# Kernel tuning notes

Measured on AMD Instinct MI355X. Metric: run time of the kernel, lower is better.

## Reference

```python
import jax, jax.numpy as jnp
import numpy as np

N = 6144          # number of agents
D = 2             # spatial dims
BOX = 100.0       # positions spread over [0, BOX)^2
DT = 0.01         # integrator timestep
MASS = 1.0
SOFT = 0.25       # softening added to r^2 to keep LJ r^-12 finite for near-coincident points


def setup_inputs() -> dict:
    key = jax.random.key(0)
    k1, k2, k3, k4 = jax.random.split(key, 4)
    pos = jax.random.uniform(k1, (N, D), dtype=jnp.float32) * BOX
    vel = jax.random.normal(k2, (N, D), dtype=jnp.float32)
    epsilon = jax.random.normal(k3, (), dtype=jnp.float32)
    sigma = jax.random.normal(k4, (), dtype=jnp.float32)
    return {"pos": pos, "vel": vel, "epsilon": epsilon, "sigma": sigma}


def reference(pos, vel, epsilon, sigma):
    # Pairwise Lennard-Jones forces (all-to-all), then one semi-implicit Euler step.
    n = pos.shape[0]
    diff = pos[:, None, :] - pos[None, :, :]          # [N, N, D]
    r2 = jnp.sum(diff * diff, axis=-1)                # [N, N]
    eye = jnp.eye(n, dtype=bool)
    r2s = jnp.where(eye, 1.0, r2 + SOFT)              # avoid div-by-zero on diagonal
    inv_r2 = (sigma * sigma) / r2s                    # (sigma/r)^2
    i6 = inv_r2 * inv_r2 * inv_r2                     # (sigma/r)^6
    # dU/dr of 4*eps*((s/r)^12 - (s/r)^6) -> force coefficient along diff
    coeff = 24.0 * epsilon * (2.0 * i6 * i6 - i6) / r2s
    coeff = jnp.where(eye, 0.0, coeff)                # no self-interaction
    force = jnp.einsum('ij,ijd->id', coeff, diff)     # [N, D]
    vel_new = vel + (DT / MASS) * force
    pos_new = pos + DT * vel_new
    return jnp.concatenate([pos_new, vel_new], axis=-1)  # [N, 2*D] world state
```

## Files before the change

kernel.cpp:

```cpp
#include <hip/hip_runtime.h>

#define NAG   6144
#define DT    0.01f
#define SOFT  0.25f

#define NJS   32
#define IPB   12
#define BLK   (NJS * IPB)
#define NBLK  (NAG / IPB)
#define JITER (NAG / (2 * NJS))

typedef __attribute__((ext_vector_type(2))) float f32x2;

__global__ __launch_bounds__(BLK, 3) void lj_fused(
    const float4* __restrict__ pos4,
    const float2* __restrict__ vel2,
    const float*  __restrict__ eps_p,
    const float*  __restrict__ sig_p,
    float4* __restrict__ out4)
{
    __shared__ __align__(16) float spx[NAG];
    __shared__ __align__(16) float spy[NAG];

    const int tid = threadIdx.x;
    for (int k = tid; k < NAG / 2; k += BLK) {
        const float4 v = pos4[k];
        *(f32x2*)&spx[2 * k] = (f32x2){v.x, v.z};
        *(f32x2*)&spy[2 * k] = (f32x2){v.y, v.w};
    }
    __syncthreads();

    const float eps  = *eps_p, s = *sig_p;
    const float s2   = s * s, s6 = s2 * s2 * s2;
    const float ke   = 24.0f * eps;
    const f32x2 ks12 = (f32x2)(2.0f * ke * s6 * s6);
    const f32x2 mks6 = (f32x2)(-ke * s6);
    const f32x2 softv = (f32x2)(SOFT);

    const int lane  = tid & 63;
    const int js    = lane & (NJS - 1);
    const int i_idx = (tid >> 6) * 2 + (lane >> 5);
    const int i     = blockIdx.x * IPB + i_idx;

    const f32x2 pix = (f32x2)(spx[i]);
    const f32x2 piy = (f32x2)(spy[i]);

    f32x2 fx = 0.f, fy = 0.f;
#pragma unroll 8
    for (int jj = 0; jj < JITER; ++jj) {
        const int j0 = jj * (2 * NJS) + 2 * js;
        const f32x2 xj = *(const f32x2*)&spx[j0];
        const f32x2 yj = *(const f32x2*)&spy[j0];
        const f32x2 dx = pix - xj, dy = piy - yj;
        const f32x2 r  = __builtin_elementwise_fma(dy, dy,
                         __builtin_elementwise_fma(dx, dx, softv));
        f32x2 u;
        u.x = __builtin_amdgcn_rcpf(r.x);
        u.y = __builtin_amdgcn_rcpf(r.y);
        const f32x2 u2 = u * u, u3 = u2 * u, u4 = u2 * u2;
        const f32x2 c  = u4 * __builtin_elementwise_fma(ks12, u3, mks6);
        fx = __builtin_elementwise_fma(c, dx, fx);
        fy = __builtin_elementwise_fma(c, dy, fy);
    }

    float sfx = fx.x + fx.y;
    float sfy = fy.x + fy.y;
#pragma unroll
    for (int m = 16; m >= 1; m >>= 1) {
        sfx += __shfl_xor(sfx, m, 64);
        sfy += __shfl_xor(sfy, m, 64);
    }

    if (js == 0) {
        const float2 v  = vel2[i];
        const float vnx = fmaf(DT, sfx, v.x);
        const float vny = fmaf(DT, sfy, v.y);
        const float pnx = fmaf(DT, vnx, spx[i]);
        const float pny = fmaf(DT, vny, spy[i]);
        out4[i] = make_float4(pnx, pny, vnx, vny);
    }
}

extern "C" void kernel_launch(void* const* d_in, const int* in_sizes, int n_in,
                              void* d_out, int out_size, void* d_ws, size_t ws_size,
                              hipStream_t stream) {
    const float4* pos4  = (const float4*)d_in[0];
    const float2* vel2  = (const float2*)d_in[1];
    const float*  eps_p = (const float*)d_in[2];
    const float*  sig_p = (const float*)d_in[3];
    float4* out4 = (float4*)d_out;
    (void)d_ws; (void)ws_size;

    lj_fused<<<NBLK, BLK, 0, stream>>>(pos4, vel2, eps_p, sig_p, out4);
}
```

Measured before the change: 18.96 us.

## Register-block two i-particles per lane and share one reciprocal per pair

Each 64-lane wavefront now computes forces for two i-agents, with every lane sweeping the full j range. Each j pair loaded from LDS is therefore reused for two i-agents, which halves LDS reads per interaction. The two per-pair reciprocals are also replaced by one rcp of r.x*r.y followed by two multiplies, cutting transcendental instructions. The cost is more registers, a longer 6-step shuffle reduction for four accumulators, and a possible overflow or precision loss in the product of r values.

```diff
diff --git a/kernel.cpp b/kernel.cpp
--- a/kernel.cpp
+++ b/kernel.cpp
@@ -4,11 +4,11 @@
 #define DT    0.01f
 #define SOFT  0.25f
 
-#define NJS   32
-#define IPB   12
-#define BLK   (NJS * IPB)
+#define BLK   384
+#define IPW   2
+#define IPB   ((BLK / 64) * IPW)
 #define NBLK  (NAG / IPB)
-#define JITER (NAG / (2 * NJS))
+#define JITER (NAG / 128)
 
 typedef __attribute__((ext_vector_type(2))) float f32x2;
 
@@ -37,47 +37,63 @@
     const f32x2 mks6 = (f32x2)(-ke * s6);
     const f32x2 softv = (f32x2)(SOFT);
 
-    const int lane  = tid & 63;
-    const int js    = lane & (NJS - 1);
-    const int i_idx = (tid >> 6) * 2 + (lane >> 5);
-    const int i     = blockIdx.x * IPB + i_idx;
+    const int lane = tid & 63;
+    const int wid  = tid >> 6;
+    const int i0   = blockIdx.x * IPB + 2 * wid;
+    const int i1   = i0 + 1;
 
-    const f32x2 pix = (f32x2)(spx[i]);
-    const f32x2 piy = (f32x2)(spy[i]);
+    const f32x2 p0x = (f32x2)(spx[i0]), p0y = (f32x2)(spy[i0]);
+    const f32x2 p1x = (f32x2)(spx[i1]), p1y = (f32x2)(spy[i1]);
 
-    f32x2 fx = 0.f, fy = 0.f;
+    f32x2 f0x = 0.f, f0y = 0.f, f1x = 0.f, f1y = 0.f;
 #pragma unroll 8
     for (int jj = 0; jj < JITER; ++jj) {
-        const int j0 = jj * (2 * NJS) + 2 * js;
+        const int j0 = jj * 128 + 2 * lane;
         const f32x2 xj = *(const f32x2*)&spx[j0];
         const f32x2 yj = *(const f32x2*)&spy[j0];
-        const f32x2 dx = pix - xj, dy = piy - yj;
-        const f32x2 r  = __builtin_elementwise_fma(dy, dy,
-                         __builtin_elementwise_fma(dx, dx, softv));
-        f32x2 u;
-        u.x = __builtin_amdgcn_rcpf(r.x);
-        u.y = __builtin_amdgcn_rcpf(r.y);
-        const f32x2 u2 = u * u, u3 = u2 * u, u4 = u2 * u2;
-        const f32x2 c  = u4 * __builtin_elementwise_fma(ks12, u3, mks6);
-        fx = __builtin_elementwise_fma(c, dx, fx);
-        fy = __builtin_elementwise_fma(c, dy, fy);
+        {
+            const f32x2 dx = p0x - xj, dy = p0y - yj;
+            const f32x2 r  = __builtin_elementwise_fma(dy, dy,
+                             __builtin_elementwise_fma(dx, dx, softv));
+            const float t  = __builtin_amdgcn_rcpf(r.x * r.y);
+            const f32x2 u  = {t * r.y, t * r.x};
+            const f32x2 u2 = u * u, u3 = u2 * u, u4 = u2 * u2;
+            const f32x2 c  = u4 * __builtin_elementwise_fma(ks12, u3, mks6);
+            f0x = __builtin_elementwise_fma(c, dx, f0x);
+            f0y = __builtin_elementwise_fma(c, dy, f0y);
+        }
+        {
+            const f32x2 dx = p1x - xj, dy = p1y - yj;
+            const f32x2 r  = __builtin_elementwise_fma(dy, dy,
+                             __builtin_elementwise_fma(dx, dx, softv));
+            const float t  = __builtin_amdgcn_rcpf(r.x * r.y);
+            const f32x2 u  = {t * r.y, t * r.x};
+            const f32x2 u2 = u * u, u3 = u2 * u, u4 = u2 * u2;
+            const f32x2 c  = u4 * __builtin_elementwise_fma(ks12, u3, mks6);
+            f1x = __builtin_elementwise_fma(c, dx, f1x);
+            f1y = __builtin_elementwise_fma(c, dy, f1y);
+        }
     }
 
-    float sfx = fx.x + fx.y;
-    float sfy = fy.x + fy.y;
+    float s0x = f0x.x + f0x.y, s0y = f0y.x + f0y.y;
+    float s1x = f1x.x + f1x.y, s1y = f1y.x + f1y.y;
 #pragma unroll
-    for (int m = 16; m >= 1; m >>= 1) {
-        sfx += __shfl_xor(sfx, m, 64);
-        sfy += __shfl_xor(sfy, m, 64);
+    for (int m = 32; m >= 1; m >>= 1) {
+        s0x += __shfl_xor(s0x, m, 64);
+        s0y += __shfl_xor(s0y, m, 64);
+        s1x += __shfl_xor(s1x, m, 64);
+        s1y += __shfl_xor(s1y, m, 64);
     }
 
-    if (js == 0) {
-        const float2 v  = vel2[i];
-        const float vnx = fmaf(DT, sfx, v.x);
-        const float vny = fmaf(DT, sfy, v.y);
-        const float pnx = fmaf(DT, vnx, spx[i]);
-        const float pny = fmaf(DT, vny, spy[i]);
-        out4[i] = make_float4(pnx, pny, vnx, vny);
+    if (lane == 0) {
+        const float2 v0 = vel2[i0];
+        const float2 v1 = vel2[i1];
+        const float vnx0 = fmaf(DT, s0x, v0.x), vny0 = fmaf(DT, s0y, v0.y);
+        const float vnx1 = fmaf(DT, s1x, v1.x), vny1 = fmaf(DT, s1y, v1.y);
+        const float pnx0 = fmaf(DT, vnx0, spx[i0]), pny0 = fmaf(DT, vny0, spy[i0]);
+        const float pnx1 = fmaf(DT, vnx1, spx[i1]), pny1 = fmaf(DT, vny1, spy[i1]);
+        out4[i0] = make_float4(pnx0, pny0, vnx0, vny0);
+        out4[i1] = make_float4(pnx1, pny1, vnx1, vny1);
     }
 }
 
```

Result: no change. 18.77 us (-1.0%).
